# Kernel tuning notes

Hardware: AMD Instinct MI355X
Metric: run time of the kernel (lower is better)

The kernel has to match this reference:

```python
import jax, jax.numpy as jnp
import numpy as np
from jax import lax

D_MODEL = 1024
N_HEADS = 16
KERNEL = 3
STRIDE = 1
PAD = 1
BATCH = 32
SEQ = D_MODEL  # required by the module's reshape: seq_len must equal d_model


def setup_inputs() -> dict:
    key = jax.random.key(0)
    k1, k2, k3, k4, k5, k6 = jax.random.split(key, 6)
    query_sequences = jax.random.normal(k1, (BATCH, SEQ, D_MODEL), dtype=jnp.float32)
    key_sequences = jax.random.normal(k2, (BATCH, SEQ, D_MODEL), dtype=jnp.float32)
    value_sequences = jax.random.normal(k3, (BATCH, SEQ, D_MODEL), dtype=jnp.float32)
    key_value_sequence_lengths = jax.random.randint(k4, (BATCH,), 0, SEQ).astype(jnp.int64)
    # nn.Linear(d_model, n_heads*kernel_size) params (stored as (in, out) for x @ W)
    scale = 1.0 / np.sqrt(D_MODEL)
    Wq = jax.random.uniform(k5, (D_MODEL, N_HEADS * KERNEL), minval=-scale, maxval=scale, dtype=jnp.float32)
    bq = jax.random.uniform(k6, (N_HEADS * KERNEL,), minval=-scale, maxval=scale, dtype=jnp.float32)
    return {
        "query_sequences": query_sequences,
        "key_sequences": key_sequences,
        "value_sequences": value_sequences,
        "key_value_sequence_lengths": key_value_sequence_lengths,
        "Wq": Wq,
        "bq": bq,
    }


def reference(query_sequences, key_sequences, value_sequences, key_value_sequence_lengths, Wq, bq):
    B, S, D = query_sequences.shape
    # per-batch dynamic conv kernels from queries: (B, S, H*K) -> (B*H, D, K)
    # (valid because S == D, mirroring the torch .view)
    qk = jnp.einsum('bsd,df->bsf', query_sequences, Wq) + bq
    kernels = qk.reshape(B * N_HEADS, D, KERNEL)
    # keys as a single grouped-conv input: (1, B*D, S)
    keys = jnp.transpose(key_sequences, (0, 2, 1)).reshape(1, B * D, S)
    # grouped conv1d with groups = batch_size (each group: in=D, out=N_HEADS)
    out = lax.conv_general_dilated(
        keys, kernels,
        window_strides=(STRIDE,),
        padding=[(PAD, PAD)],
        dimension_numbers=('NCH', 'OIH', 'NCH'),
        feature_group_count=B,
    )
    return out.reshape(B, N_HEADS, S)
```

## Files before the change

### kernel.cpp

```cpp
#include <hip/hip_runtime.h>
#include <hip/hip_bf16.h>
#include <stdint.h>

typedef __attribute__((ext_vector_type(8))) short bf16x8;
typedef __attribute__((ext_vector_type(4))) float f32x4;

__device__ __forceinline__ short f2bf(float x) {
    uint32_t u = __builtin_bit_cast(uint32_t, x);
    uint32_t r = (u + 0x7FFFu + ((u >> 16) & 1u)) >> 16;
    return (short)r;
}

__device__ __forceinline__ bf16x8 pack8(f32x4 a, f32x4 b) {
    bf16x8 r;
    r[0] = f2bf(a[0]); r[1] = f2bf(a[1]); r[2] = f2bf(a[2]); r[3] = f2bf(a[3]);
    r[4] = f2bf(b[0]); r[5] = f2bf(b[1]); r[6] = f2bf(b[2]); r[7] = f2bf(b[3]);
    return r;
}

__global__ __launch_bounds__(256) void prep_wfrag(const float* __restrict__ Wq,
                                                  short* __restrict__ wfrag) {
    int idx = blockIdx.x * 256 + threadIdx.x;
    int j    = idx & 7;
    int lane = (idx >> 3) & 63;
    int grp  = idx >> 9;
    int nf   = grp % 3;
    int ks   = grp / 3;
    int k = ks * 32 + ((lane >> 4) << 3) + j;
    int n = nf * 16 + (lane & 15);
    wfrag[idx] = f2bf(Wq[k * 48 + n]);
}

__global__ __launch_bounds__(256) void qk_gemm(const float* __restrict__ Q,
                                               const short* __restrict__ wfrag,
                                               const float* __restrict__ bq,
                                               short* __restrict__ wgtA) {
    const int l  = threadIdx.x & 63;
    const int w  = threadIdx.x >> 6;
    const int lr = l & 15;
    const int lk = l >> 4;
    const int row0 = blockIdx.x * 64 + w * 16;

    f32x4 acc[3];
    acc[0] = (f32x4){0.f, 0.f, 0.f, 0.f};
    acc[1] = acc[0];
    acc[2] = acc[0];

    const float* qbase = Q + (size_t)(row0 + lr) * 1024 + lk * 8;

    #pragma unroll 4
    for (int ks = 0; ks < 32; ++ks) {
        const float* p = qbase + ks * 32;
        f32x4 q0 = *(const f32x4*)p;
        f32x4 q1 = *(const f32x4*)(p + 4);
        bf16x8 a = pack8(q0, q1);
        const bf16x8* wp = (const bf16x8*)(wfrag + (size_t)ks * 1536 + l * 8);
        acc[0] = __builtin_amdgcn_mfma_f32_16x16x32_bf16(a, wp[0],   acc[0], 0, 0, 0);
        acc[1] = __builtin_amdgcn_mfma_f32_16x16x32_bf16(a, wp[64],  acc[1], 0, 0, 0);
        acc[2] = __builtin_amdgcn_mfma_f32_16x16x32_bf16(a, wp[128], acc[2], 0, 0, 0);
    }

    #pragma unroll
    for (int nf = 0; nf < 3; ++nf) {
        int n = nf * 16 + lr;
        float bias = bq[n];
        int t  = n / 3;
        int kk = n - t * 3;
        #pragma unroll
        for (int r = 0; r < 4; ++r) {
            int row = row0 + lk * 4 + r;
            int b   = row >> 10;
            int h   = (row >> 6) & 15;
            int sp  = row & 63;
            int dg  = sp * 2 + (t >> 3);
            int j   = t & 7;
            wgtA[(((size_t)(b * 3 + kk) * 128 + dg) << 7) + h * 8 + j] = f2bf(acc[nf][r] + bias);
        }
    }
}

__global__ __launch_bounds__(256, 4) void conv_mfma(const float* __restrict__ Key,
                                                    const short* __restrict__ wgtA,
                                                    float* __restrict__ out) {
    __shared__ short klds[2][66][72];
    const int blk = blockIdx.x;
    const int kc  = blk & 1;
    const int st  = (blk >> 1) & 15;
    const int b   = blk >> 5;
    const int s0  = st << 6;
    const int tid = threadIdx.x;
    const int l   = tid & 63;
    const int w   = tid >> 6;
    const int lr  = l & 15;
    const int lk  = l >> 4;

    const float* keyB = Key + ((size_t)b << 20) + (kc << 9);
    const short* wgtW = wgtA + (((size_t)b * 384 + (kc << 6)) << 7) + lk * 128 + lr * 8;

    const int j8 = tid & 7;
    const int r0 = tid >> 3;
    const int srow0 = s0 - 1 + r0;
    const int srow1 = s0 + 31 + r0;
    const int srow2 = s0 + 63 + r0;
    const bool ok0 = (srow0 >= 0);
    const bool ok2 = (tid < 16) && (srow2 < 1024);
    const f32x4* q0 = (const f32x4*)(keyB + (size_t)(ok0 ? srow0 : 0) * 1024 + j8 * 8);
    const f32x4* q1 = (const f32x4*)(keyB + (size_t)srow1 * 1024 + j8 * 8);
    const f32x4* q2 = (const f32x4*)(keyB + (size_t)(ok2 ? srow2 : 0) * 1024 + j8 * 8);

    const f32x4 z4 = (f32x4){0.f, 0.f, 0.f, 0.f};
    f32x4 vA0, vA1, vB0, vB1, vC0, vC1;

    vA0 = ok0 ? q0[0] : z4;  vA1 = ok0 ? q0[1] : z4;
    vB0 = q1[0];             vB1 = q1[1];
    vC0 = ok2 ? q2[0] : z4;  vC1 = ok2 ? q2[1] : z4;
    *(bf16x8*)&klds[0][r0][j8 * 8]      = pack8(vA0, vA1);
    *(bf16x8*)&klds[0][r0 + 32][j8 * 8] = pack8(vB0, vB1);
    if (tid < 16) *(bf16x8*)&klds[0][64 + r0][j8 * 8] = pack8(vC0, vC1);
    __syncthreads();

    f32x4 acc = z4;

    #pragma unroll 2
    for (int c = 0; c < 8; ++c) {
        const int buf = c & 1;
        const bool pre = (c + 1 < 8);
        if (pre) {
            const int o = (c + 1) * 16;
            vA0 = ok0 ? q0[o] : z4;  vA1 = ok0 ? q0[o + 1] : z4;
            vB0 = q1[o];             vB1 = q1[o + 1];
            vC0 = ok2 ? q2[o] : z4;  vC1 = ok2 ? q2[o + 1] : z4;
        }
        #pragma unroll
        for (int k = 0; k < 3; ++k) {
            #pragma unroll
            for (int d2 = 0; d2 < 2; ++d2) {
                bf16x8 a  = *(const bf16x8*)(wgtW + (size_t)k * 16384 + (c * 8 + d2 * 4) * 128);
                bf16x8 kv = *(const bf16x8*)(&klds[buf][w * 16 + lr + k][d2 * 32 + lk * 8]);
                acc = __builtin_amdgcn_mfma_f32_16x16x32_bf16(a, kv, acc, 0, 0, 0);
            }
        }
        __syncthreads();
        if (pre) {
            *(bf16x8*)&klds[buf ^ 1][r0][j8 * 8]      = pack8(vA0, vA1);
            *(bf16x8*)&klds[buf ^ 1][r0 + 32][j8 * 8] = pack8(vB0, vB1);
            if (tid < 16) *(bf16x8*)&klds[buf ^ 1][64 + r0][j8 * 8] = pack8(vC0, vC1);
            __syncthreads();
        }
    }

    const int s = s0 + w * 16 + lr;
    #pragma unroll
    for (int r = 0; r < 4; ++r) {
        int h = lk * 4 + r;
        atomicAdd(&out[(((b << 4) + h) << 10) + s], acc[r]);
    }
}

extern "C" void kernel_launch(void* const* d_in, const int* in_sizes, int n_in,
                              void* d_out, int out_size, void* d_ws, size_t ws_size,
                              hipStream_t stream) {
    const float* Q  = (const float*)d_in[0];
    const float* K  = (const float*)d_in[1];
    const float* Wq = (const float*)d_in[4];
    const float* bq = (const float*)d_in[5];
    float* outp = (float*)d_out;

    short* wfrag = (short*)d_ws;
    short* wgtA  = (short*)((char*)d_ws + 98304);

    hipMemsetAsync(outp, 0, (size_t)out_size * sizeof(float), stream);
    hipLaunchKernelGGL(prep_wfrag, dim3(192),  dim3(256), 0, stream, Wq, wfrag);
    hipLaunchKernelGGL(qk_gemm,    dim3(512),  dim3(256), 0, stream, Q, wfrag, bq, wgtA);
    hipLaunchKernelGGL(conv_mfma,  dim3(1024), dim3(256), 0, stream, K, wgtA, outp);
}
```

Measured before the change: 66.81 us.

## Split conv channel reduction four ways and pack before barrier

The conv kernel's channel dimension is now split into four chunks instead of two, doubling the grid to 2048 blocks with half the loop trips each. The occupancy hint is raised to 6 blocks per SM and the loop is fully unrolled. Bf16 packing of the prefetched keys now happens before the barrier, and f2bf uses the library conversion. The extra parallelism is meant to fill the GPU better and hide memory latency, at the cost of twice as many atomic adds to the output and more redundant halo-row loads.

```diff
diff --git a/kernel.cpp b/kernel.cpp
--- a/kernel.cpp
+++ b/kernel.cpp
@@ -6,9 +6,8 @@
 typedef __attribute__((ext_vector_type(4))) float f32x4;
 
 __device__ __forceinline__ short f2bf(float x) {
-    uint32_t u = __builtin_bit_cast(uint32_t, x);
-    uint32_t r = (u + 0x7FFFu + ((u >> 16) & 1u)) >> 16;
-    return (short)r;
+    __hip_bfloat16 h = __float2bfloat16(x);
+    return __builtin_bit_cast(short, h);
 }
 
 __device__ __forceinline__ bf16x8 pack8(f32x4 a, f32x4 b) {
@@ -79,14 +78,14 @@
     }
 }
 
-__global__ __launch_bounds__(256, 4) void conv_mfma(const float* __restrict__ Key,
+__global__ __launch_bounds__(256, 6) void conv_mfma(const float* __restrict__ Key,
                                                     const short* __restrict__ wgtA,
                                                     float* __restrict__ out) {
     __shared__ short klds[2][66][72];
     const int blk = blockIdx.x;
-    const int kc  = blk & 1;
-    const int st  = (blk >> 1) & 15;
-    const int b   = blk >> 5;
+    const int kc  = blk & 3;
+    const int st  = (blk >> 2) & 15;
+    const int b   = blk >> 6;
     const int s0  = st << 6;
     const int tid = threadIdx.x;
     const int l   = tid & 63;
@@ -94,8 +93,8 @@
     const int lr  = l & 15;
     const int lk  = l >> 4;
 
-    const float* keyB = Key + ((size_t)b << 20) + (kc << 9);
-    const short* wgtW = wgtA + (((size_t)b * 384 + (kc << 6)) << 7) + lk * 128 + lr * 8;
+    const float* keyB = Key + ((size_t)b << 20) + (kc << 8);
+    const short* wgtW = wgtA + (((size_t)b * 384 + (kc << 5)) << 7) + lk * 128 + lr * 8;
 
     const int j8 = tid & 7;
     const int r0 = tid >> 3;
@@ -109,27 +108,29 @@
     const f32x4* q2 = (const f32x4*)(keyB + (size_t)(ok2 ? srow2 : 0) * 1024 + j8 * 8);
 
     const f32x4 z4 = (f32x4){0.f, 0.f, 0.f, 0.f};
-    f32x4 vA0, vA1, vB0, vB1, vC0, vC1;
 
-    vA0 = ok0 ? q0[0] : z4;  vA1 = ok0 ? q0[1] : z4;
-    vB0 = q1[0];             vB1 = q1[1];
-    vC0 = ok2 ? q2[0] : z4;  vC1 = ok2 ? q2[1] : z4;
-    *(bf16x8*)&klds[0][r0][j8 * 8]      = pack8(vA0, vA1);
-    *(bf16x8*)&klds[0][r0 + 32][j8 * 8] = pack8(vB0, vB1);
-    if (tid < 16) *(bf16x8*)&klds[0][64 + r0][j8 * 8] = pack8(vC0, vC1);
+    {
+        f32x4 a0 = ok0 ? q0[0] : z4, a1 = ok0 ? q0[1] : z4;
+        f32x4 b0 = q1[0],            b1 = q1[1];
+        f32x4 c0 = ok2 ? q2[0] : z4, c1 = ok2 ? q2[1] : z4;
+        *(bf16x8*)&klds[0][r0][j8 * 8]      = pack8(a0, a1);
+        *(bf16x8*)&klds[0][r0 + 32][j8 * 8] = pack8(b0, b1);
+        if (tid < 16) *(bf16x8*)&klds[0][64 + r0][j8 * 8] = pack8(c0, c1);
+    }
     __syncthreads();
 
     f32x4 acc = z4;
 
-    #pragma unroll 2
-    for (int c = 0; c < 8; ++c) {
+    #pragma unroll
+    for (int c = 0; c < 4; ++c) {
         const int buf = c & 1;
-        const bool pre = (c + 1 < 8);
+        const bool pre = (c + 1 < 4);
+        f32x4 a0, a1, b0, b1, c0, c1;
         if (pre) {
             const int o = (c + 1) * 16;
-            vA0 = ok0 ? q0[o] : z4;  vA1 = ok0 ? q0[o + 1] : z4;
-            vB0 = q1[o];             vB1 = q1[o + 1];
-            vC0 = ok2 ? q2[o] : z4;  vC1 = ok2 ? q2[o + 1] : z4;
+            a0 = ok0 ? q0[o] : z4;  a1 = ok0 ? q0[o + 1] : z4;
+            b0 = q1[o];             b1 = q1[o + 1];
+            c0 = ok2 ? q2[o] : z4;  c1 = ok2 ? q2[o + 1] : z4;
         }
         #pragma unroll
         for (int k = 0; k < 3; ++k) {
@@ -140,11 +141,14 @@
                 acc = __builtin_amdgcn_mfma_f32_16x16x32_bf16(a, kv, acc, 0, 0, 0);
             }
         }
-        __syncthreads();
         if (pre) {
-            *(bf16x8*)&klds[buf ^ 1][r0][j8 * 8]      = pack8(vA0, vA1);
-            *(bf16x8*)&klds[buf ^ 1][r0 + 32][j8 * 8] = pack8(vB0, vB1);
-            if (tid < 16) *(bf16x8*)&klds[buf ^ 1][64 + r0][j8 * 8] = pack8(vC0, vC1);
+            bf16x8 wA = pack8(a0, a1);
+            bf16x8 wB = pack8(b0, b1);
+            bf16x8 wC = pack8(c0, c1);
+            __syncthreads();
+            *(bf16x8*)&klds[buf ^ 1][r0][j8 * 8]      = wA;
+            *(bf16x8*)&klds[buf ^ 1][r0 + 32][j8 * 8] = wB;
+            if (tid < 16) *(bf16x8*)&klds[buf ^ 1][64 + r0][j8 * 8] = wC;
             __syncthreads();
         }
     }
@@ -172,5 +176,5 @@
     hipMemsetAsync(outp, 0, (size_t)out_size * sizeof(float), stream);
     hipLaunchKernelGGL(prep_wfrag, dim3(192),  dim3(256), 0, stream, Wq, wfrag);
     hipLaunchKernelGGL(qk_gemm,    dim3(512),  dim3(256), 0, stream, Q, wfrag, bq, wgtA);
-    hipLaunchKernelGGL(conv_mfma,  dim3(1024), dim3(256), 0, stream, K, wgtA, outp);
+    hipLaunchKernelGGL(conv_mfma,  dim3(2048), dim3(256), 0, stream, K, wgtA, outp);
 }
```

Result: no change. 66.44 us (-0.6%).
